# Optimization experiments

Hardware: AMD Instinct MI355X
Metric: run time of the kernel (lower is better)

Reference implementation:

```python
import jax, jax.numpy as jnp
import numpy as np

B, L, D_IN, H, N_BLOCKS, N_STATE, PRED = 2048, 168, 9, 96, 4, 96, 96
N2 = N_STATE // 2  # complex-conjugate pairs: keep half the state, double the real part


def s4d_kernel(log_dt, log_A_real, A_imag, C_re, C_im, length):
    # S4D (diagonal SSM) convolution kernel, ZOH-style discretization.
    dt = jnp.exp(log_dt)[:, None]                  # (H,1)
    A = -jnp.exp(log_A_real) + 1j * A_imag         # (H,N2)
    C = C_re + 1j * C_im                           # (H,N2)
    dtA = dt * A                                   # (H,N2)
    Ct = C * (jnp.exp(dtA) - 1.0) / A              # discretized C
    # Vandermonde: K[h,l] = 2*Re(sum_n Ct[h,n] * exp(dtA[h,n] * l))
    V = jnp.exp(dtA[:, :, None] * jnp.arange(length))  # (H,N2,L)
    return 2.0 * jnp.einsum('hn,hnl->hl', Ct, V).real  # (H,L)


def causal_conv(u, K):
    # u: (B,L,H), K: (H,L) -> causal depthwise convolution via FFT
    n = 2 * u.shape[1]
    Uf = jnp.fft.rfft(u, n=n, axis=1)              # (B,n/2+1,H)
    Kf = jnp.fft.rfft(K.T, n=n, axis=0)            # (n/2+1,H)
    return jnp.fft.irfft(Uf * Kf[None], n=n, axis=1)[:, :u.shape[1]]


def layer_norm(x, w, b):
    mu = x.mean(-1, keepdims=True)
    var = x.var(-1, keepdims=True)
    return (x - mu) / jnp.sqrt(var + 1e-5) * w + b


def setup_inputs() -> dict:
    key = jax.random.key(0)
    ks = jax.random.split(key, 20)
    r = lambda k, s, sc=1.0: jax.random.normal(k, s, jnp.float32) * sc
    inp = {
        'x': r(ks[0], (B, L, D_IN)),
        'enc_W': r(ks[1], (D_IN, H), 1.0 / np.sqrt(D_IN)),
        'enc_b': jnp.zeros((H,), jnp.float32),
        # per-block S4D parameters, stacked on leading n_blocks axis
        'log_dt': jax.random.uniform(ks[2], (N_BLOCKS, H), jnp.float32,
                                     np.log(1e-3), np.log(1e-1)),
        'log_A_real': jnp.full((N_BLOCKS, H, N2), np.log(0.5), jnp.float32),
        'A_imag': jnp.tile(np.pi * jnp.arange(N2, dtype=jnp.float32), (N_BLOCKS, H, 1)),
        'C_re': r(ks[3], (N_BLOCKS, H, N2), 0.5),
        'C_im': r(ks[4], (N_BLOCKS, H, N2), 0.5),
        'D_skip': r(ks[5], (N_BLOCKS, H)),
        'W_out': r(ks[6], (N_BLOCKS, H, H), 1.0 / np.sqrt(H)),
        'b_out': jnp.zeros((N_BLOCKS, H), jnp.float32),
        'ln_w': jnp.ones((N_BLOCKS, H), jnp.float32),
        'ln_b': jnp.zeros((N_BLOCKS, H), jnp.float32),
        'dec_W': r(ks[7], (H, H), 1.0 / np.sqrt(H)),
        'dec_b': jnp.zeros((H,), jnp.float32),
        'fc1_W': r(ks[8], (H * L, H), 1.0 / np.sqrt(H * L)),
        'fc1_b': jnp.zeros((H,), jnp.float32),
        'fc2_W': r(ks[9], (H, PRED), 1.0 / np.sqrt(H)),
        'fc2_b': jnp.zeros((PRED,), jnp.float32),
    }
    return inp


def reference(x, enc_W, enc_b, log_dt, log_A_real, A_imag, C_re, C_im, D_skip,
              W_out, b_out, ln_w, ln_b, dec_W, dec_b, fc1_W, fc1_b, fc2_W, fc2_b):
    h = x @ enc_W + enc_b                              # (B,L,H) encoder
    for i in range(N_BLOCKS):                          # post-norm residual S4 blocks
        K = s4d_kernel(log_dt[i], log_A_real[i], A_imag[i], C_re[i], C_im[i], L)
        z = causal_conv(h, K) + h * D_skip[i]          # SSM conv + skip D*u
        z = jax.nn.gelu(z)                             # activation (dropout off at eval)
        z = z @ W_out[i] + b_out[i]                    # output mixing
        h = layer_norm(h + z, ln_w[i], ln_b[i])        # residual + post-norm
    h = h @ dec_W + dec_b                              # S4Model decoder (d_model->d_model)
    out = h.reshape(h.shape[0], -1) @ fc1_W + fc1_b    # flatten + fc1
    out = out @ fc2_W + fc2_b                          # fc2 -> PRED_LEN
    return out[..., None]                              # (B,96,1)
```

## Files before the change

### kernel.cpp

```cpp
#include <hip/hip_runtime.h>
#include <hip/hip_bf16.h>
#include <math.h>

#define NB 4
#define B  2048
#define L  168
#define DI 9
#define H  96
#define N2 48

#define ZSTR2 132

typedef short short8 __attribute__((ext_vector_type(8)));
typedef float f32x4  __attribute__((ext_vector_type(4)));
typedef unsigned short u16x8 __attribute__((ext_vector_type(8)));
typedef unsigned short u16x4 __attribute__((ext_vector_type(4)));

__device__ __forceinline__ float gelu_f(float x) {
    float x3 = x * x * x;
    float y  = 0.7978845608028654f * (x + 0.044715f * x3);
    float ey = __expf(2.0f * y);
    float t  = 1.0f - 2.0f / (ey + 1.0f);
    return 0.5f * x * (1.0f + t);
}

__device__ __forceinline__ unsigned short bf16_rne(float x) {
    unsigned u = __float_as_uint(x);
    return (unsigned short)((u + 0x7FFFu + ((u >> 16) & 1u)) >> 16);
}
__device__ __forceinline__ float b2f(unsigned short v) {
    return __uint_as_float((unsigned)v << 16);
}

__global__ void kgen_kernel(const float* __restrict__ log_dt, const float* __restrict__ lar,
                            const float* __restrict__ aim, const float* __restrict__ cre,
                            const float* __restrict__ cim, float* __restrict__ K)
{
    const int ih   = blockIdx.x;
    const int lane = threadIdx.x;
    float ctre = 0.f, ctim = 0.f, pre = 0.f, pim = 0.f, mre = 0.f, mim = 0.f;
    if (lane < N2) {
        float dt  = expf(log_dt[ih]);
        int   idx = ih * N2 + lane;
        float reA = -expf(lar[idx]);
        float imA = aim[idx];
        float dre = dt * reA, dim = dt * imA;
        float er  = expf(dre);
        float sv, cv;
        sincosf(dim, &sv, &cv);
        mre = er * cv; mim = er * sv;
        float nre = mre - 1.0f, nim = mim;
        float den = reA * reA + imA * imA;
        float tre = (nre * reA + nim * imA) / den;
        float tim = (nim * reA - nre * imA) / den;
        float cr = cre[idx], ci = cim[idx];
        ctre = cr * tre - ci * tim;
        ctim = cr * tim + ci * tre;
        pre = 1.0f; pim = 0.0f;
    }
    float* Kr = K + ih * L;
    for (int l = 0; l < L; ++l) {
        float term = ctre * pre - ctim * pim;
        #pragma unroll
        for (int off = 32; off > 0; off >>= 1) term += __shfl_xor(term, off, 64);
        if (lane == 0) Kr[l] = 2.0f * term;
        float nr = pre * mre - pim * mim;
        float ni = pre * mim + pim * mre;
        pre = nr; pim = ni;
    }
}

__global__ void wprep_kernel(const float* __restrict__ wout, short* __restrict__ wfrag, int ntask)
{
    int idx = blockIdx.x * 256 + threadIdx.x;
    if (idx >= ntask) return;
    int layer = idx / 9216;  int rem  = idx - layer * 9216;
    int ch    = rem / 3072;  int rem2 = rem - ch * 3072;
    int m     = rem2 / 512;  int rem3 = rem2 - m * 512;
    int s     = rem3 / 256;  int rem4 = rem3 - s * 256;
    int lane  = rem4 / 4;    int d    = rem4 - lane * 4;
    int g = lane >> 4, c = lane & 15;
    int k  = ch * 32 + g * 8 + 2 * d;
    int hp = m * 16 + c;
    const float* Wl = wout + (size_t)layer * H * H;
    float w0 = Wl[k * H + hp];
    float w1 = Wl[(k + 1) * H + hp];
    unsigned short b0, b1;
    if (s == 0) { b0 = bf16_rne(w0); b1 = bf16_rne(w1); }
    else {
        unsigned short h0 = bf16_rne(w0), h1 = bf16_rne(w1);
        b0 = bf16_rne(w0 - b2f(h0));
        b1 = bf16_rne(w1 - b2f(h1));
    }
    wfrag[idx * 2]     = (short)b0;
    wfrag[idx * 2 + 1] = (short)b1;
}

__global__ void tgen_kernel(const float* __restrict__ Kg, short* __restrict__ tfrag)
{
    static const int kmaxA[11] = {0, 0, 1, 1, 2, 2, 3, 3, 4, 4, 5};
    static const int toffA[11] = {0, 1, 2, 4, 6, 9, 12, 16, 20, 25, 30};
    int idx = blockIdx.x * 256 + threadIdx.x;
    if (idx >= 96 * 66 * 64) return;
    int lane = idx & 63;
    int t    = (idx >> 6) % 66;
    int h    = (idx >> 6) / 66;
    int mi = t / 6, ki = t - mi * 6;
    if (ki > kmaxA[mi]) return;
    int g = lane >> 4, c = lane & 15;
    int row = mi * 16 + c;
    short8 a;
    #pragma unroll
    for (int j = 0; j < 8; ++j) {
        int kk = ki * 32 + g * 8 + j;
        int d  = row - kk;
        float val = (row < L && d >= 0) ? Kg[h * L + d] : 0.0f;
        a[j] = (short)bf16_rne(val);
    }
    short8* dst = (short8*)tfrag + (size_t)(h * 36 + toffA[mi] + ki) * 64;
    dst[lane] = a;
}

__launch_bounds__(256)
__global__ void wcomp_kernel(const float* __restrict__ decW, const float* __restrict__ decb,
                             const float* __restrict__ fc1W, float* __restrict__ wcs,
                             float* __restrict__ cbpart)
{
    __shared__ float Bs[96 * 100];
    const int tid = threadIdx.x;
    const int l   = blockIdx.x;
    for (int e = tid; e < 96 * 96; e += 256) {
        int h = e / 96, p = e - h * 96;
        Bs[h * 100 + p] = fc1W[(size_t)(l * 96 + h) * 96 + p];
    }
    __syncthreads();
    const int pt = tid & 31;
    const int kt = tid >> 5;
    float acc[12][3];
    #pragma unroll
    for (int kk = 0; kk < 12; ++kk)
        #pragma unroll
        for (int j = 0; j < 3; ++j) acc[kk][j] = 0.f;
    for (int h = 0; h < 96; ++h) {
        float dw[12];
        #pragma unroll
        for (int kk = 0; kk < 12; ++kk) dw[kk] = decW[(kt + 8 * kk) * 96 + h];
        float bs[3];
        #pragma unroll
        for (int j = 0; j < 3; ++j) bs[j] = Bs[h * 100 + pt + 32 * j];
        #pragma unroll
        for (int kk = 0; kk < 12; ++kk)
            #pragma unroll
            for (int j = 0; j < 3; ++j) acc[kk][j] = fmaf(dw[kk], bs[j], acc[kk][j]);
    }
    float* wl = wcs + (size_t)l * 9216;
    #pragma unroll
    for (int kk = 0; kk < 12; ++kk)
        #pragma unroll
        for (int j = 0; j < 3; ++j)
            wl[(kt + 8 * kk) * 96 + pt + 32 * j] = acc[kk][j];
    if (kt == 0) {
        #pragma unroll
        for (int j = 0; j < 3; ++j) {
            float s = 0.f;
            for (int h = 0; h < 96; ++h) s = fmaf(decb[h], Bs[h * 100 + pt + 32 * j], s);
            cbpart[l * 96 + pt + 32 * j] = s;
        }
    }
}

__global__ void cbias_red_kernel(const float* __restrict__ cbpart, const float* __restrict__ fc1b,
                                 float* __restrict__ cbias)
{
    int p = threadIdx.x;
    if (p < 96) {
        float s = fc1b[p];
        for (int l = 0; l < L; ++l) s += cbpart[l * 96 + p];
        cbias[p] = s;
    }
}

__launch_bounds__(256)
__global__ void enc2_kernel(const float* __restrict__ x, const float* __restrict__ W,
                            const float* __restrict__ bias, unsigned short* __restrict__ hb2)
{
    __shared__ float Ws[DI * H];
    __shared__ float bs[H];
    const int tid = threadIdx.x;
    const int l   = blockIdx.x;
    const int b0  = blockIdx.y * 256;
    for (int e = tid; e < DI * H; e += 256) Ws[e] = W[e];
    if (tid < H) bs[tid] = bias[tid];
    __syncthreads();
    float xv[DI];
    const float* xr = x + (size_t)(b0 + tid) * (L * DI) + l * DI;
    #pragma unroll
    for (int k = 0; k < DI; ++k) xv[k] = xr[k];
    for (int h = 0; h < H; ++h) {
        float a = bs[h];
        #pragma unroll
        for (int k = 0; k < DI; ++k) a = fmaf(xv[k], Ws[k * H + h], a);
        hb2[((size_t)h * L + l) * B + b0 + tid] = bf16_rne(a);
    }
}

__launch_bounds__(512)
__global__ void conv3_kernel(const unsigned short* __restrict__ hb2, const short* __restrict__ tfrag,
                             const float* __restrict__ Dsk, unsigned short* __restrict__ z2)
{
    static const int toffA[11] = {0, 1, 2, 4, 6, 9, 12, 16, 20, 25, 30};
    __shared__ __align__(16) unsigned short zs[192 * ZSTR2];
    const int tid  = threadIdx.x;
    const int w    = tid >> 6;
    const int lane = tid & 63;
    const int g    = lane >> 4;
    const int cc   = lane & 15;
    const int h    = blockIdx.x;
    const int b0   = blockIdx.y * 128;

    for (int e = tid; e < 168 * 16; e += 512) {
        int lp = e >> 4, b8 = e & 15;
        u16x8 v = *(const u16x8*)(hb2 + ((size_t)h * L + lp) * B + b0 + b8 * 8);
        *(u16x4*)(&zs[lp * ZSTR2 + b8 * 8])     = (u16x4){v[0], v[1], v[2], v[3]};
        *(u16x4*)(&zs[lp * ZSTR2 + b8 * 8 + 4]) = (u16x4){v[4], v[5], v[6], v[7]};
    }
    for (int e = tid; e < 24 * 16; e += 512) {
        int lp = 168 + (e >> 4), b8 = e & 15;
        *(u16x4*)(&zs[lp * ZSTR2 + b8 * 8])     = (u16x4){0, 0, 0, 0};
        *(u16x4*)(&zs[lp * ZSTR2 + b8 * 8 + 4]) = (u16x4){0, 0, 0, 0};
    }
    __syncthreads();

    f32x4 acc[11];
    #pragma unroll
    for (int mi = 0; mi < 11; ++mi) acc[mi] = (f32x4){0.f, 0.f, 0.f, 0.f};

    const int col = w * 16 + cc;

    #pragma unroll
    for (int ki = 0; ki < 6; ++ki) {
        short8 bh;
        #pragma unroll
        for (int j = 0; j < 8; ++j)
            bh[j] = (short)zs[(ki * 32 + g * 8 + j) * ZSTR2 + col];
        #pragma unroll
        for (int mi = 2 * ki; mi < 11; ++mi) {
            const short8* Tf = (const short8*)(tfrag) + (size_t)(h * 36 + toffA[mi] + ki) * 64;
            short8 ah = Tf[lane];
            acc[mi] = __builtin_amdgcn_mfma_f32_16x16x32_bf16(ah, bh, acc[mi], 0, 0, 0);
        }
    }

    const float ds = Dsk[h];
    #pragma unroll
    for (int mi = 0; mi < 11; ++mi) {
        #pragma unroll
        for (int r = 0; r < 4; ++r) {
            int l = mi * 16 + g * 4 + r;
            if (l < L) {
                float uu = b2f(zs[l * ZSTR2 + col]);
                float zv = gelu_f(fmaf(ds, uu, acc[mi][r]));
                z2[((size_t)h * L + l) * B + b0 + col] = bf16_rne(zv);
            }
        }
    }
}

__launch_bounds__(256)
__global__ void mix2_kernel(const unsigned short* __restrict__ z2, unsigned short* __restrict__ hb2,
                            const short* __restrict__ wfrag, const float* __restrict__ bout,
                            const float* __restrict__ lnw, const float* __restrict__ lnb)
{
    __shared__ __align__(16) unsigned short zs[H * ZSTR2];
    const int tid  = threadIdx.x;
    const int w    = tid >> 6;
    const int lane = tid & 63;
    const int g    = lane >> 4;
    const int cc   = lane & 15;
    const int l    = blockIdx.x;
    const int b0   = blockIdx.y * 128;

    for (int e = tid; e < 96 * 16; e += 256) {
        int hh = e >> 4, b8 = e & 15;
        u16x8 v = *(const u16x8*)(z2 + ((size_t)hh * L + l) * B + b0 + b8 * 8);
        *(u16x4*)(&zs[hh * ZSTR2 + b8 * 8])     = (u16x4){v[0], v[1], v[2], v[3]};
        *(u16x4*)(&zs[hh * ZSTR2 + b8 * 8 + 4]) = (u16x4){v[4], v[5], v[6], v[7]};
    }
    __syncthreads();

    f32x4 acc[2][6];
    #pragma unroll
    for (int n2 = 0; n2 < 2; ++n2)
        #pragma unroll
        for (int m = 0; m < 6; ++m) acc[n2][m] = (f32x4){0.f, 0.f, 0.f, 0.f};

    for (int ks = 0; ks < 3; ++ks) {
        short8 bh[2];
        #pragma unroll
        for (int n2 = 0; n2 < 2; ++n2) {
            int col = (w * 2 + n2) * 16 + cc;
            #pragma unroll
            for (int j = 0; j < 8; ++j)
                bh[n2][j] = (short)zs[(ks * 32 + g * 8 + j) * ZSTR2 + col];
        }
        const short8* Wf = (const short8*)(wfrag) + ks * 12 * 64;
        #pragma unroll
        for (int m = 0; m < 6; ++m) {
            short8 ah = Wf[(m * 2 + 0) * 64 + lane];
            short8 al = Wf[(m * 2 + 1) * 64 + lane];
            #pragma unroll
            for (int n2 = 0; n2 < 2; ++n2) {
                acc[n2][m] = __builtin_amdgcn_mfma_f32_16x16x32_bf16(al, bh[n2], acc[n2][m], 0, 0, 0);
                acc[n2][m] = __builtin_amdgcn_mfma_f32_16x16x32_bf16(ah, bh[n2], acc[n2][m], 0, 0, 0);
            }
        }
    }

    #pragma unroll
    for (int n2 = 0; n2 < 2; ++n2) {
        int gb = b0 + (w * 2 + n2) * 16 + cc;
        float vals[6][4];
        float s = 0.f, q = 0.f;
        #pragma unroll
        for (int m = 0; m < 6; ++m) {
            float4 B4 = *(const float4*)(bout + m * 16 + g * 4);
            float bo[4] = {B4.x, B4.y, B4.z, B4.w};
            #pragma unroll
            for (int r = 0; r < 4; ++r) {
                int hr = m * 16 + g * 4 + r;
                float res = b2f(hb2[((size_t)hr * L + l) * B + gb]);
                float v = acc[n2][m][r] + bo[r] + res;
                vals[m][r] = v;
                s += v; q += v * v;
            }
        }
        s += __shfl_xor(s, 16, 64); q += __shfl_xor(q, 16, 64);
        s += __shfl_xor(s, 32, 64); q += __shfl_xor(q, 32, 64);
        float mean = s * (1.0f / 96.0f);
        float var  = q * (1.0f / 96.0f) - mean * mean;
        float rstd = rsqrtf(var + 1e-5f);
        #pragma unroll
        for (int m = 0; m < 6; ++m) {
            float4 W4 = *(const float4*)(lnw + m * 16 + g * 4);
            float4 Bb = *(const float4*)(lnb + m * 16 + g * 4);
            float wv[4] = {W4.x, W4.y, W4.z, W4.w};
            float bv[4] = {Bb.x, Bb.y, Bb.z, Bb.w};
            #pragma unroll
            for (int r = 0; r < 4; ++r) {
                int hr = m * 16 + g * 4 + r;
                hb2[((size_t)hr * L + l) * B + gb] =
                    bf16_rne(fmaf((vals[m][r] - mean) * rstd, wv[r], bv[r]));
            }
        }
    }
}

__launch_bounds__(256)
__global__ void fc1m_kernel(const unsigned short* __restrict__ hb2, const short* __restrict__ wcfrag,
                            float* __restrict__ partial)
{
    __shared__ __align__(16) unsigned short zs[H * ZSTR2];
    const int tid  = threadIdx.x;
    const int w    = tid >> 6;
    const int lane = tid & 63;
    const int g    = lane >> 4;
    const int cc   = lane & 15;
    const int ksp  = blockIdx.x;
    const int b0   = blockIdx.y * 128;

    f32x4 acc[2][6];
    #pragma unroll
    for (int n2 = 0; n2 < 2; ++n2)
        #pragma unroll
        for (int m = 0; m < 6; ++m) acc[n2][m] = (f32x4){0.f, 0.f, 0.f, 0.f};

    for (int il = 0; il < 4; ++il) {
        const int l = ksp * 4 + il;
        __syncthreads();
        for (int e = tid; e < 96 * 16; e += 256) {
            int hh = e >> 4, b8 = e & 15;
            u16x8 v = *(const u16x8*)(hb2 + ((size_t)hh * L + l) * B + b0 + b8 * 8);
            *(u16x4*)(&zs[hh * ZSTR2 + b8 * 8])     = (u16x4){v[0], v[1], v[2], v[3]};
            *(u16x4*)(&zs[hh * ZSTR2 + b8 * 8 + 4]) = (u16x4){v[4], v[5], v[6], v[7]};
        }
        __syncthreads();
        for (int ksl = 0; ksl < 3; ++ksl) {
            short8 bh[2];
            #pragma unroll
            for (int n2 = 0; n2 < 2; ++n2) {
                int col = (w * 2 + n2) * 16 + cc;
                #pragma unroll
                for (int j = 0; j < 8; ++j)
                    bh[n2][j] = (short)zs[(ksl * 32 + g * 8 + j) * ZSTR2 + col];
            }
            const short8* Wf = (const short8*)(wcfrag) + (size_t)(l * 3 + ksl) * 768;
            #pragma unroll
            for (int m = 0; m < 6; ++m) {
                short8 ah = Wf[(m * 2 + 0) * 64 + lane];
                short8 al = Wf[(m * 2 + 1) * 64 + lane];
                #pragma unroll
                for (int n2 = 0; n2 < 2; ++n2) {
                    acc[n2][m] = __builtin_amdgcn_mfma_f32_16x16x32_bf16(al, bh[n2], acc[n2][m], 0, 0, 0);
                    acc[n2][m] = __builtin_amdgcn_mfma_f32_16x16x32_bf16(ah, bh[n2], acc[n2][m], 0, 0, 0);
                }
            }
        }
    }

    #pragma unroll
    for (int n2 = 0; n2 < 2; ++n2) {
        int gb = b0 + (w * 2 + n2) * 16 + cc;
        #pragma unroll
        for (int m = 0; m < 6; ++m) {
            *(float4*)&partial[((size_t)ksp * B + gb) * 96 + m * 16 + g * 4] =
                make_float4(acc[n2][m][0], acc[n2][m][1], acc[n2][m][2], acc[n2][m][3]);
        }
    }
}

__global__ void fc1red_kernel(const float* __restrict__ partial, const float* __restrict__ cbias,
                              float* __restrict__ t1)
{
    int o = blockIdx.x * 256 + threadIdx.x;
    int p = o % 96;
    float s = cbias[p];
    #pragma unroll 6
    for (int k = 0; k < 42; ++k) s += partial[(size_t)k * (B * 96) + o];
    t1[o] = s;
}

__launch_bounds__(256)
__global__ void fc2_kernel(const float* __restrict__ t1, const float* __restrict__ W,
                           const float* __restrict__ fb, float* __restrict__ out)
{
    __shared__ float Ws[96 * 100];
    const int tid = threadIdx.x;
    for (int e = tid; e < 96 * 96; e += 256) Ws[(e / 96) * 100 + (e % 96)] = W[e];
    __syncthreads();
    int o = blockIdx.x * 256 + tid;
    int b = o / 96, p = o - b * 96;
    const float* tr = t1 + b * 96;
    float acc = fb[p];
    #pragma unroll 4
    for (int h = 0; h < 96; ++h) acc = fmaf(tr[h], Ws[h * 100 + p], acc);
    out[o] = acc;
}

extern "C" void kernel_launch(void* const* d_in, const int* in_sizes, int n_in,
                              void* d_out, int out_size, void* d_ws, size_t ws_size,
                              hipStream_t stream)
{
    const float* x      = (const float*)d_in[0];
    const float* encW   = (const float*)d_in[1];
    const float* encb   = (const float*)d_in[2];
    const float* log_dt = (const float*)d_in[3];
    const float* lar    = (const float*)d_in[4];
    const float* aim    = (const float*)d_in[5];
    const float* cre    = (const float*)d_in[6];
    const float* cim    = (const float*)d_in[7];
    const float* dsk    = (const float*)d_in[8];
    const float* wout   = (const float*)d_in[9];
    const float* boutp  = (const float*)d_in[10];
    const float* lnw    = (const float*)d_in[11];
    const float* lnb    = (const float*)d_in[12];
    const float* decW   = (const float*)d_in[13];
    const float* decb   = (const float*)d_in[14];
    const float* fc1W   = (const float*)d_in[15];
    const float* fc1b   = (const float*)d_in[16];
    const float* fc2W   = (const float*)d_in[17];
    const float* fc2b   = (const float*)d_in[18];

    char*           ws      = (char*)d_ws;
    float*          K       = (float*)(ws);
    short*          wfrag   = (short*)(ws + ((size_t)384 << 10));
    float*          t1      = (float*)(ws + ((size_t)1 << 20));
    float*          cbpart  = (float*)(ws + ((size_t)1 << 20) + (900 << 10));
    float*          cbias   = (float*)(ws + ((size_t)1 << 20) + (980 << 10));
    short*          wcfrag  = (short*)(ws + ((size_t)2 << 20));
    short*          tfrag   = (short*)(ws + ((size_t)9 << 20));
    float*          wcs     = (float*)(ws + ((size_t)9 << 20));
    unsigned short* hb2     = (unsigned short*)(ws + ((size_t)16 << 20));
    unsigned short* z2      = (unsigned short*)(ws + ((size_t)80 << 20));
    float*          partial = (float*)(ws + ((size_t)80 << 20));

    kgen_kernel<<<NB * H, 64, 0, stream>>>(log_dt, lar, aim, cre, cim, K);
    wprep_kernel<<<144, 256, 0, stream>>>(wout, wfrag, NB * 9216);
    wcomp_kernel<<<L, 256, 0, stream>>>(decW, decb, fc1W, wcs, cbpart);
    wprep_kernel<<<6048, 256, 0, stream>>>(wcs, wcfrag, L * 9216);
    cbias_red_kernel<<<1, 128, 0, stream>>>(cbpart, fc1b, cbias);
    enc2_kernel<<<dim3(L, 8), 256, 0, stream>>>(x, encW, encb, hb2);
    for (int i = 0; i < NB; ++i) {
        tgen_kernel<<<1584, 256, 0, stream>>>(K + i * H * L, tfrag);
        conv3_kernel<<<dim3(H, 16), 512, 0, stream>>>(hb2, tfrag, dsk + i * H, z2);
        mix2_kernel<<<dim3(L, 16), 256, 0, stream>>>(z2, hb2, wfrag + i * 18432,
                                                     boutp + i * H, lnw + i * H, lnb + i * H);
    }
    fc1m_kernel<<<dim3(42, 16), 256, 0, stream>>>(hb2, wcfrag, partial);
    fc1red_kernel<<<768, 256, 0, stream>>>(partial, cbias, t1);
    fc2_kernel<<<768, 256, 0, stream>>>(t1, fc2W, fc2b, (float*)d_out);
}
```

Measured before the change: 569.4 us.

## Stage conv and mix outputs through LDS for coalesced 16-byte global stores

The conv kernel now writes its GELU results back into its shared tile and then stores them to global memory as coalesced 16-byte vectors, replacing scattered 2-byte stores. The mix kernel moves to 512 threads with one 16-column slice per wave. It stages the residual hb2 tile in a second shared buffer, builds the layer-normed output there, and writes it back with vectorised coalesced stores. This targets the strided 2-byte global reads and writes in both kernels, at the cost of doubling mix's shared memory and adding extra barriers.

After: 569.6 us. About the same (+0.0%).

```diff
diff --git a/kernel.cpp b/kernel.cpp
--- a/kernel.cpp
+++ b/kernel.cpp
@@ -260,18 +260,27 @@
             if (l < L) {
                 float uu = b2f(zs[l * ZSTR2 + col]);
                 float zv = gelu_f(fmaf(ds, uu, acc[mi][r]));
-                z2[((size_t)h * L + l) * B + b0 + col] = bf16_rne(zv);
+                zs[l * ZSTR2 + col] = bf16_rne(zv);
             }
         }
     }
-}
-
-__launch_bounds__(256)
+    __syncthreads();
+    for (int e = tid; e < 168 * 16; e += 512) {
+        int lp = e >> 4, b8 = e & 15;
+        u16x4 a = *(const u16x4*)(&zs[lp * ZSTR2 + b8 * 8]);
+        u16x4 b = *(const u16x4*)(&zs[lp * ZSTR2 + b8 * 8 + 4]);
+        u16x8 v = {a[0], a[1], a[2], a[3], b[0], b[1], b[2], b[3]};
+        *(u16x8*)(z2 + ((size_t)h * L + lp) * B + b0 + b8 * 8) = v;
+    }
+}
+
+__launch_bounds__(512)
 __global__ void mix2_kernel(const unsigned short* __restrict__ z2, unsigned short* __restrict__ hb2,
                             const short* __restrict__ wfrag, const float* __restrict__ bout,
                             const float* __restrict__ lnw, const float* __restrict__ lnb)
 {
     __shared__ __align__(16) unsigned short zs[H * ZSTR2];
+    __shared__ __align__(16) unsigned short rs[H * ZSTR2];
     const int tid  = threadIdx.x;
     const int w    = tid >> 6;
     const int lane = tid & 63;
@@ -280,78 +289,81 @@
     const int l    = blockIdx.x;
     const int b0   = blockIdx.y * 128;
 
-    for (int e = tid; e < 96 * 16; e += 256) {
+    for (int e = tid; e < 96 * 16; e += 512) {
         int hh = e >> 4, b8 = e & 15;
         u16x8 v = *(const u16x8*)(z2 + ((size_t)hh * L + l) * B + b0 + b8 * 8);
         *(u16x4*)(&zs[hh * ZSTR2 + b8 * 8])     = (u16x4){v[0], v[1], v[2], v[3]};
         *(u16x4*)(&zs[hh * ZSTR2 + b8 * 8 + 4]) = (u16x4){v[4], v[5], v[6], v[7]};
     }
-    __syncthreads();
-
-    f32x4 acc[2][6];
-    #pragma unroll
-    for (int n2 = 0; n2 < 2; ++n2)
-        #pragma unroll
-        for (int m = 0; m < 6; ++m) acc[n2][m] = (f32x4){0.f, 0.f, 0.f, 0.f};
-
+    for (int e = tid; e < 96 * 16; e += 512) {
+        int hh = e >> 4, b8 = e & 15;
+        u16x8 v = *(const u16x8*)(hb2 + ((size_t)hh * L + l) * B + b0 + b8 * 8);
+        *(u16x4*)(&rs[hh * ZSTR2 + b8 * 8])     = (u16x4){v[0], v[1], v[2], v[3]};
+        *(u16x4*)(&rs[hh * ZSTR2 + b8 * 8 + 4]) = (u16x4){v[4], v[5], v[6], v[7]};
+    }
+    __syncthreads();
+
+    f32x4 acc[6];
+    #pragma unroll
+    for (int m = 0; m < 6; ++m) acc[m] = (f32x4){0.f, 0.f, 0.f, 0.f};
+
+    const int col = w * 16 + cc;
+
+    #pragma unroll
     for (int ks = 0; ks < 3; ++ks) {
-        short8 bh[2];
-        #pragma unroll
-        for (int n2 = 0; n2 < 2; ++n2) {
-            int col = (w * 2 + n2) * 16 + cc;
-            #pragma unroll
-            for (int j = 0; j < 8; ++j)
-                bh[n2][j] = (short)zs[(ks * 32 + g * 8 + j) * ZSTR2 + col];
-        }
+        short8 bh;
+        #pragma unroll
+        for (int j = 0; j < 8; ++j)
+            bh[j] = (short)zs[(ks * 32 + g * 8 + j) * ZSTR2 + col];
         const short8* Wf = (const short8*)(wfrag) + ks * 12 * 64;
         #pragma unroll
         for (int m = 0; m < 6; ++m) {
             short8 ah = Wf[(m * 2 + 0) * 64 + lane];
             short8 al = Wf[(m * 2 + 1) * 64 + lane];
-            #pragma unroll
-            for (int n2 = 0; n2 < 2; ++n2) {
-                acc[n2][m] = __builtin_amdgcn_mfma_f32_16x16x32_bf16(al, bh[n2], acc[n2][m], 0, 0, 0);
-                acc[n2][m] = __builtin_amdgcn_mfma_f32_16x16x32_bf16(ah, bh[n2], acc[n2][m], 0, 0, 0);
-            }
-        }
-    }
-
-    #pragma unroll
-    for (int n2 = 0; n2 < 2; ++n2) {
-        int gb = b0 + (w * 2 + n2) * 16 + cc;
-        float vals[6][4];
-        float s = 0.f, q = 0.f;
-        #pragma unroll
-        for (int m = 0; m < 6; ++m) {
-            float4 B4 = *(const float4*)(bout + m * 16 + g * 4);
-            float bo[4] = {B4.x, B4.y, B4.z, B4.w};
-            #pragma unroll
-            for (int r = 0; r < 4; ++r) {
-                int hr = m * 16 + g * 4 + r;
-                float res = b2f(hb2[((size_t)hr * L + l) * B + gb]);
-                float v = acc[n2][m][r] + bo[r] + res;
-                vals[m][r] = v;
-                s += v; q += v * v;
-            }
-        }
-        s += __shfl_xor(s, 16, 64); q += __shfl_xor(q, 16, 64);
-        s += __shfl_xor(s, 32, 64); q += __shfl_xor(q, 32, 64);
-        float mean = s * (1.0f / 96.0f);
-        float var  = q * (1.0f / 96.0f) - mean * mean;
-        float rstd = rsqrtf(var + 1e-5f);
-        #pragma unroll
-        for (int m = 0; m < 6; ++m) {
-            float4 W4 = *(const float4*)(lnw + m * 16 + g * 4);
-            float4 Bb = *(const float4*)(lnb + m * 16 + g * 4);
-            float wv[4] = {W4.x, W4.y, W4.z, W4.w};
-            float bv[4] = {Bb.x, Bb.y, Bb.z, Bb.w};
-            #pragma unroll
-            for (int r = 0; r < 4; ++r) {
-                int hr = m * 16 + g * 4 + r;
-                hb2[((size_t)hr * L + l) * B + gb] =
-                    bf16_rne(fmaf((vals[m][r] - mean) * rstd, wv[r], bv[r]));
-            }
-        }
+            acc[m] = __builtin_amdgcn_mfma_f32_16x16x32_bf16(al, bh, acc[m], 0, 0, 0);
+            acc[m] = __builtin_amdgcn_mfma_f32_16x16x32_bf16(ah, bh, acc[m], 0, 0, 0);
+        }
+    }
+
+    float vals[6][4];
+    float s = 0.f, q = 0.f;
+    #pragma unroll
+    for (int m = 0; m < 6; ++m) {
+        float4 B4 = *(const float4*)(bout + m * 16 + g * 4);
+        float bo[4] = {B4.x, B4.y, B4.z, B4.w};
+        #pragma unroll
+        for (int r = 0; r < 4; ++r) {
+            int hr = m * 16 + g * 4 + r;
+            float res = b2f(rs[hr * ZSTR2 + col]);
+            float v = acc[m][r] + bo[r] + res;
+            vals[m][r] = v;
+            s += v; q += v * v;
+        }
+    }
+    s += __shfl_xor(s, 16, 64); q += __shfl_xor(q, 16, 64);
+    s += __shfl_xor(s, 32, 64); q += __shfl_xor(q, 32, 64);
+    float mean = s * (1.0f / 96.0f);
+    float var  = q * (1.0f / 96.0f) - mean * mean;
+    float rstd = rsqrtf(var + 1e-5f);
+    #pragma unroll
+    for (int m = 0; m < 6; ++m) {
+        float4 W4 = *(const float4*)(lnw + m * 16 + g * 4);
+        float4 Bb = *(const float4*)(lnb + m * 16 + g * 4);
+        float wv[4] = {W4.x, W4.y, W4.z, W4.w};
+        float bv[4] = {Bb.x, Bb.y, Bb.z, Bb.w};
+        #pragma unroll
+        for (int r = 0; r < 4; ++r) {
+            int hr = m * 16 + g * 4 + r;
+            rs[hr * ZSTR2 + col] = bf16_rne(fmaf((vals[m][r] - mean) * rstd, wv[r], bv[r]));
+        }
+    }
+    __syncthreads();
+    for (int e = tid; e < 96 * 16; e += 512) {
+        int hh = e >> 4, b8 = e & 15;
+        u16x4 a = *(const u16x4*)(&rs[hh * ZSTR2 + b8 * 8]);
+        u16x4 b = *(const u16x4*)(&rs[hh * ZSTR2 + b8 * 8 + 4]);
+        u16x8 v = {a[0], a[1], a[2], a[3], b[0], b[1], b[2], b[3]};
+        *(u16x8*)(hb2 + ((size_t)hh * L + l) * B + b0 + b8 * 8) = v;
     }
 }
 
@@ -492,7 +504,7 @@
     for (int i = 0; i < NB; ++i) {
         tgen_kernel<<<1584, 256, 0, stream>>>(K + i * H * L, tfrag);
         conv3_kernel<<<dim3(H, 16), 512, 0, stream>>>(hb2, tfrag, dsk + i * H, z2);
-        mix2_kernel<<<dim3(L, 16), 256, 0, stream>>>(z2, hb2, wfrag + i * 18432,
+        mix2_kernel<<<dim3(L, 16), 512, 0, stream>>>(z2, hb2, wfrag + i * 18432,
                                                      boutp + i * H, lnw + i * H, lnb + i * H);
     }
     fc1m_kernel<<<dim3(42, 16), 256, 0, stream>>>(hb2, wcfrag, partial);
```
